# Kernel tuning notes

Measured on AMD Instinct MI355X. Metric: run time of the kernel, lower is better.

Reference implementation:

```python
import jax, jax.numpy as jnp
import numpy as np

TEXT_SIZE = 1024
HIDDEN = 512

def setup_inputs() -> dict:
    key = jax.random.key(0)
    k1, k2, k3, k4, k5, k6 = jax.random.split(key, 6)
    B, S, D, H = 32, 4096, TEXT_SIZE, HIDDEN
    text_seq = jax.random.normal(k1, (B, S, D), dtype=jnp.float32)
    previous_hidden = jax.random.normal(k2, (B, D), dtype=jnp.float32)
    # attention_hidden: Linear(D -> H) + ReLU
    W1 = jax.random.normal(k3, (D, H), dtype=jnp.float32) / np.sqrt(D)
    b1 = jax.random.normal(k4, (H,), dtype=jnp.float32) * 0.01
    # attention_scoring: Linear(H -> 1)
    w2 = jax.random.normal(k5, (H,), dtype=jnp.float32) / np.sqrt(H)
    b2 = jax.random.normal(k6, (), dtype=jnp.float32) * 0.01
    return {"text_seq": text_seq, "previous_hidden": previous_hidden,
            "W1": W1, "b1": b1, "w2": w2, "b2": b2}

def reference(text_seq, previous_hidden, W1, b1, w2, b2):
    # text_seq: [B, S, D]; previous_hidden: [B, D]
    # per-timestep: score = Linear1(ReLU(Linear0(prev * h_t))) -> batched here
    prod = text_seq * previous_hidden[:, None, :]          # [B, S, D]
    hidden = jax.nn.relu(jnp.einsum('bsd,dh->bsh', prod, W1) + b1)  # [B, S, H]
    scores = jnp.einsum('bsh,h->bs', hidden, w2) + b2      # [B, S]
    weights = jax.nn.softmax(scores, axis=1)               # [B, S]
    out = jnp.einsum('bsd,bs->bd', text_seq, weights)      # [B, D]
    return out
```

## Files before the change

### kernel.cpp

```cpp
#include <hip/hip_runtime.h>
#include <hip/hip_bf16.h>
#include <stdint.h>

#define B_ 32
#define S_ 4096
#define D_ 1024
#define H_ 512
#define BK 32
#define NCHUNK 64

typedef __bf16 bf16_t;
typedef bf16_t bf16x8 __attribute__((ext_vector_type(8)));
typedef float f32x4 __attribute__((ext_vector_type(4)));

#define AS_STRIDE 40

__global__ __launch_bounds__(256)
void ta_prep_kernel(const float* __restrict__ W1, bf16_t* __restrict__ W1bf)
{
    const int kb = blockIdx.x;
    const int t  = threadIdx.x;

#pragma unroll
    for (int hh = 0; hh < 2; ++hh) {
        int h = t + hh * 256;
        bf16_t row[BK];
#pragma unroll
        for (int kk = 0; kk < BK; ++kk)
            row[kk] = (bf16_t)W1[(size_t)(kb * BK + kk) * H_ + h];
        bf16_t* dst = W1bf + ((size_t)kb * H_ + h) * BK;
#pragma unroll
        for (int c = 0; c < 4; ++c)
            *(bf16x8*)(dst + c * 8) = *(const bf16x8*)&row[c * 8];
    }
}

__global__ __launch_bounds__(256, 2)
void ta_fused_kernel(const float* __restrict__ x,
                     const float* __restrict__ prev,
                     const bf16_t* __restrict__ W1bf,
                     const float* __restrict__ b1,
                     const float* __restrict__ w2,
                     const float* __restrict__ b2,
                     float* __restrict__ pout,
                     float* __restrict__ mlbuf)
{
    __shared__ bf16_t As[64 * AS_STRIDE];
    __shared__ bf16_t Bs[H_ * BK];
    __shared__ float  scoreS[4][64];
    __shared__ float  wS[64];

    const int t    = threadIdx.x;
    const int wv   = t >> 6;
    const int lane = t & 63;
    const int quad = lane >> 4;
    const int n16  = lane & 15;

    const int b  = blockIdx.y;
    const int s0 = blockIdx.x * 64;

    const int ar = t >> 2;
    const int ac = (t & 3) * 8;
    const float* xrow  = x + ((size_t)b * S_ + s0 + ar) * D_;
    const float* prevb = prev + (size_t)b * D_;

    float b1v[8], w2v[8];
#pragma unroll
    for (int j = 0; j < 8; ++j) {
        int h = wv * 128 + j * 16 + n16;
        b1v[j] = b1[h];
        w2v[j] = w2[h];
    }

    f32x4 acc[4][8];
#pragma unroll
    for (int i = 0; i < 4; ++i)
#pragma unroll
        for (int j = 0; j < 8; ++j)
            acc[i][j] = (f32x4){0.f, 0.f, 0.f, 0.f};

    for (int kb = 0; kb < D_ / BK; ++kb) {
        f32x4 a0 = *(const f32x4*)(xrow + kb * BK + ac);
        f32x4 a1 = *(const f32x4*)(xrow + kb * BK + ac + 4);
        f32x4 p0 = *(const f32x4*)(prevb + kb * BK + ac);
        f32x4 p1 = *(const f32x4*)(prevb + kb * BK + ac + 4);

        __syncthreads();

        const char* gB = (const char*)(W1bf + (size_t)kb * H_ * BK);
#pragma unroll
        for (int r = 0; r < 8; ++r) {
            int off = (wv * 8 + r) * 1024;
            __builtin_amdgcn_global_load_lds(
                (const __attribute__((address_space(1))) void*)(gB + off + lane * 16),
                (__attribute__((address_space(3))) void*)((char*)Bs + off),
                16, 0, 0);
        }

        {
            a0 *= p0;
            a1 *= p1;
            bf16x8 aw;
#pragma unroll
            for (int e = 0; e < 4; ++e) { aw[e] = (bf16_t)a0[e]; aw[4 + e] = (bf16_t)a1[e]; }
            *(bf16x8*)&As[ar * AS_STRIDE + ac] = aw;
        }

        __syncthreads();

        bf16x8 afr[4];
#pragma unroll
        for (int i = 0; i < 4; ++i)
            afr[i] = *(const bf16x8*)&As[(i * 16 + n16) * AS_STRIDE + quad * 8];
#pragma unroll
        for (int j = 0; j < 8; ++j) {
            bf16x8 bfr = *(const bf16x8*)&Bs[(wv * 128 + j * 16 + n16) * BK + quad * 8];
#pragma unroll
            for (int i = 0; i < 4; ++i)
                acc[i][j] = __builtin_amdgcn_mfma_f32_16x16x32_bf16(afr[i], bfr, acc[i][j], 0, 0, 0);
        }
    }

    float part[4][4];
#pragma unroll
    for (int i = 0; i < 4; ++i)
#pragma unroll
        for (int r = 0; r < 4; ++r) {
            float p = 0.f;
#pragma unroll
            for (int j = 0; j < 8; ++j) {
                float hval = acc[i][j][r] + b1v[j];
                hval = fmaxf(hval, 0.f);
                p += hval * w2v[j];
            }
            for (int off = 8; off > 0; off >>= 1)
                p += __shfl_xor(p, off);
            part[i][r] = p;
        }

    if (n16 == 0) {
#pragma unroll
        for (int i = 0; i < 4; ++i)
#pragma unroll
            for (int r = 0; r < 4; ++r)
                scoreS[wv][i * 16 + quad * 4 + r] = part[i][r];
    }
    __syncthreads();

    if (t < 64) {
        float sc = scoreS[0][t] + scoreS[1][t] + scoreS[2][t] + scoreS[3][t] + b2[0];
        float m = sc;
#pragma unroll
        for (int off = 32; off > 0; off >>= 1)
            m = fmaxf(m, __shfl_xor(m, off));
        float wexp = __expf(sc - m);
        float l = wexp;
#pragma unroll
        for (int off = 32; off > 0; off >>= 1)
            l += __shfl_xor(l, off);
        wS[t] = wexp;
        if (t == 0) {
            float* ml = mlbuf + ((size_t)b * NCHUNK + blockIdx.x) * 2;
            ml[0] = m;
            ml[1] = l;
        }
    }
    __syncthreads();

    const float* xb = x + ((size_t)b * S_ + s0) * D_;
    f32x4 acc0 = (f32x4){0.f,0.f,0.f,0.f}, acc1 = acc0, acc2 = acc0, acc3 = acc0;
    for (int s = 0; s < 64; s += 4) {
        f32x4 x0 = *(const f32x4*)(xb + (size_t)(s + 0) * D_ + t * 4);
        f32x4 x1 = *(const f32x4*)(xb + (size_t)(s + 1) * D_ + t * 4);
        f32x4 x2 = *(const f32x4*)(xb + (size_t)(s + 2) * D_ + t * 4);
        f32x4 x3 = *(const f32x4*)(xb + (size_t)(s + 3) * D_ + t * 4);
        acc0 += x0 * wS[s + 0];
        acc1 += x1 * wS[s + 1];
        acc2 += x2 * wS[s + 2];
        acc3 += x3 * wS[s + 3];
    }
    f32x4 r = (acc0 + acc1) + (acc2 + acc3);
    *(f32x4*)(pout + ((size_t)b * NCHUNK + blockIdx.x) * D_ + t * 4) = r;
}

__global__ __launch_bounds__(256)
void ta_combine_kernel(const float* __restrict__ pout,
                       const float* __restrict__ mlbuf,
                       float* __restrict__ out)
{
    const int b = blockIdx.y;
    const int t = threadIdx.x;
    const int d = blockIdx.x * 256 + t;

    __shared__ float scaleS[NCHUNK];
    if (t < NCHUNK) {
        const float* ml = mlbuf + ((size_t)b * NCHUNK + t) * 2;
        float m = ml[0];
        float l = ml[1];
        float M = m;
#pragma unroll
        for (int off = 32; off > 0; off >>= 1)
            M = fmaxf(M, __shfl_xor(M, off));
        float le = l * __expf(m - M);
        float L = le;
#pragma unroll
        for (int off = 32; off > 0; off >>= 1)
            L += __shfl_xor(L, off);
        scaleS[t] = __expf(m - M) / L;
    }
    __syncthreads();

    const float* pb = pout + (size_t)b * NCHUNK * D_ + d;
    float a0 = 0.f, a1 = 0.f, a2 = 0.f, a3 = 0.f;
#pragma unroll 4
    for (int c = 0; c < NCHUNK; c += 4) {
        a0 += pb[(size_t)(c + 0) * D_] * scaleS[c + 0];
        a1 += pb[(size_t)(c + 1) * D_] * scaleS[c + 1];
        a2 += pb[(size_t)(c + 2) * D_] * scaleS[c + 2];
        a3 += pb[(size_t)(c + 3) * D_] * scaleS[c + 3];
    }
    out[(size_t)b * D_ + d] = (a0 + a1) + (a2 + a3);
}

extern "C" void kernel_launch(void* const* d_in, const int* in_sizes, int n_in,
                              void* d_out, int out_size, void* d_ws, size_t ws_size,
                              hipStream_t stream) {
    const float* x    = (const float*)d_in[0];
    const float* prev = (const float*)d_in[1];
    const float* W1   = (const float*)d_in[2];
    const float* b1   = (const float*)d_in[3];
    const float* w2   = (const float*)d_in[4];
    const float* b2   = (const float*)d_in[5];
    float* out = (float*)d_out;

    bf16_t* W1bf  = (bf16_t*)d_ws;
    float*  pout  = (float*)((char*)d_ws + (size_t)1 * 1024 * 1024);
    float*  mlbuf = (float*)((char*)d_ws + (size_t)9 * 1024 * 1024);

    ta_prep_kernel<<<32, 256, 0, stream>>>(W1, W1bf);

    dim3 g1(NCHUNK, B_);
    ta_fused_kernel<<<g1, 256, 0, stream>>>(x, prev, W1bf, b1, w2, b2, pout, mlbuf);

    dim3 g2(D_ / 256, B_);
    ta_combine_kernel<<<g2, 256, 0, stream>>>(pout, mlbuf, out);
}
```

Measured before the change: 838.8 us.

## Double-buffer A/B tiles and prefetch x two steps ahead in fused GEMM

Restructures the K-loop into a software pipeline. A and B LDS tiles are double-buffered, the next W1 tile is issued via global_load_lds while MFMAs run on the current one, and x rows are register-prefetched two iterations ahead. prev is staged once in shared memory instead of reloaded from global each step, and one barrier per iteration replaces two. This raises LDS use, which may limit occupancy, and adds hand-written waitcnt/barrier asm that must match the load counts.

After: 830.6 us. Within noise of the previous version (-1.0%).

```diff
diff --git a/kernel.cpp b/kernel.cpp
--- a/kernel.cpp
+++ b/kernel.cpp
@@ -45,8 +45,9 @@
                      float* __restrict__ pout,
                      float* __restrict__ mlbuf)
 {
-    __shared__ bf16_t As[64 * AS_STRIDE];
-    __shared__ bf16_t Bs[H_ * BK];
+    __shared__ bf16_t As[2][64 * AS_STRIDE];
+    __shared__ bf16_t Bs[2][H_ * BK];
+    __shared__ float  prevS[D_];
     __shared__ float  scoreS[4][64];
     __shared__ float  wS[64];
 
@@ -64,61 +65,106 @@
     const float* xrow  = x + ((size_t)b * S_ + s0 + ar) * D_;
     const float* prevb = prev + (size_t)b * D_;
 
+    f32x4 acc[4][8];
+#pragma unroll
+    for (int i = 0; i < 4; ++i)
+#pragma unroll
+        for (int j = 0; j < 8; ++j)
+            acc[i][j] = (f32x4){0.f, 0.f, 0.f, 0.f};
+
+    *(f32x4*)&prevS[t * 4] = *(const f32x4*)(prevb + t * 4);
+
+    f32x4 xA0 = *(const f32x4*)(xrow + ac);
+    f32x4 xA1 = *(const f32x4*)(xrow + ac + 4);
+
+    {
+        const char* gB = (const char*)W1bf;
+#pragma unroll
+        for (int r = 0; r < 8; ++r) {
+            int off = (wv * 8 + r) * 1024;
+            __builtin_amdgcn_global_load_lds(
+                (const __attribute__((address_space(1))) void*)(gB + off + lane * 16),
+                (__attribute__((address_space(3))) void*)((char*)Bs[0] + off),
+                16, 0, 0);
+        }
+    }
+    __syncthreads();
+
+    {
+        f32x4 pv0 = *(const f32x4*)&prevS[ac];
+        f32x4 pv1 = *(const f32x4*)&prevS[ac + 4];
+        f32x4 sc0 = xA0 * pv0, sc1 = xA1 * pv1;
+        bf16x8 aw;
+#pragma unroll
+        for (int e = 0; e < 4; ++e) { aw[e] = (bf16_t)sc0[e]; aw[4 + e] = (bf16_t)sc1[e]; }
+        *(bf16x8*)&As[0][ar * AS_STRIDE + ac] = aw;
+    }
+    f32x4 xB0 = *(const f32x4*)(xrow + BK + ac);
+    f32x4 xB1 = *(const f32x4*)(xrow + BK + ac + 4);
+
+    asm volatile("s_waitcnt lgkmcnt(0)\n\ts_barrier" ::: "memory");
+
+#define TA_BODY(KB, CBUF, XU0, XU1, XN0, XN1)                                    \
+    {                                                                            \
+        const int kb_ = (KB);                                                    \
+        bf16x8 afr[4];                                                           \
+        _Pragma("unroll")                                                        \
+        for (int i = 0; i < 4; ++i)                                              \
+            afr[i] = *(const bf16x8*)&As[CBUF][(i * 16 + n16) * AS_STRIDE + quad * 8]; \
+               \
+        {                                                                        \
+            const int kp = (kb_ + 1 < 32) ? kb_ + 1 : 31;                        \
+            f32x4 pv0 = *(const f32x4*)&prevS[kp * BK + ac];                     \
+            f32x4 pv1 = *(const f32x4*)&prevS[kp * BK + ac + 4];                 \
+            f32x4 sc0 = XU0 * pv0, sc1 = XU1 * pv1;                              \
+            bf16x8 aw;                                                           \
+            _Pragma("unroll")                                                    \
+            for (int e = 0; e < 4; ++e) { aw[e] = (bf16_t)sc0[e]; aw[4 + e] = (bf16_t)sc1[e]; } \
+            *(bf16x8*)&As[(CBUF) ^ 1][ar * AS_STRIDE + ac] = aw;                 \
+        }                                                                        \
+                       \
+        {                                                                        \
+            const int kp = (kb_ + 1 < 32) ? kb_ + 1 : 31;                        \
+            const char* gB = (const char*)(W1bf + (size_t)kp * H_ * BK);         \
+            char* lB = (char*)Bs[(CBUF) ^ 1];                                    \
+            _Pragma("unroll")                                                    \
+            for (int r = 0; r < 8; ++r) {                                        \
+                int off = (wv * 8 + r) * 1024;                                   \
+                __builtin_amdgcn_global_load_lds(                                \
+                    (const __attribute__((address_space(1))) void*)(gB + off + lane * 16), \
+                    (__attribute__((address_space(3))) void*)(lB + off), 16, 0, 0); \
+            }                                                                    \
+        }                                                                        \
+                    \
+        {                                                                        \
+            const int kp2 = (kb_ + 2 < 32) ? kb_ + 2 : 31;                       \
+            XN0 = *(const f32x4*)(xrow + kp2 * BK + ac);                         \
+            XN1 = *(const f32x4*)(xrow + kp2 * BK + ac + 4);                     \
+        }                                                                        \
+                \
+        _Pragma("unroll")                                                        \
+        for (int j = 0; j < 8; ++j) {                                            \
+            bf16x8 bfr = *(const bf16x8*)&Bs[CBUF][(wv * 128 + j * 16 + n16) * BK + quad * 8]; \
+            _Pragma("unroll")                                                    \
+            for (int i = 0; i < 4; ++i)                                          \
+                acc[i][j] = __builtin_amdgcn_mfma_f32_16x16x32_bf16(afr[i], bfr, acc[i][j], 0, 0, 0); \
+        }                                                                        \
+                    \
+        asm volatile("s_waitcnt vmcnt(2) lgkmcnt(0)\n\ts_barrier" ::: "memory"); \
+    }
+
+    for (int kb2 = 0; kb2 < 32; kb2 += 2) {
+        TA_BODY(kb2,     0, xB0, xB1, xA0, xA1);
+        TA_BODY(kb2 + 1, 1, xA0, xA1, xB0, xB1);
+    }
+#undef TA_BODY
+
     float b1v[8], w2v[8];
 #pragma unroll
     for (int j = 0; j < 8; ++j) {
         int h = wv * 128 + j * 16 + n16;
         b1v[j] = b1[h];
         w2v[j] = w2[h];
-    }
-
-    f32x4 acc[4][8];
-#pragma unroll
-    for (int i = 0; i < 4; ++i)
-#pragma unroll
-        for (int j = 0; j < 8; ++j)
-            acc[i][j] = (f32x4){0.f, 0.f, 0.f, 0.f};
-
-    for (int kb = 0; kb < D_ / BK; ++kb) {
-        f32x4 a0 = *(const f32x4*)(xrow + kb * BK + ac);
-        f32x4 a1 = *(const f32x4*)(xrow + kb * BK + ac + 4);
-        f32x4 p0 = *(const f32x4*)(prevb + kb * BK + ac);
-        f32x4 p1 = *(const f32x4*)(prevb + kb * BK + ac + 4);
-
-        __syncthreads();
-
-        const char* gB = (const char*)(W1bf + (size_t)kb * H_ * BK);
-#pragma unroll
-        for (int r = 0; r < 8; ++r) {
-            int off = (wv * 8 + r) * 1024;
-            __builtin_amdgcn_global_load_lds(
-                (const __attribute__((address_space(1))) void*)(gB + off + lane * 16),
-                (__attribute__((address_space(3))) void*)((char*)Bs + off),
-                16, 0, 0);
-        }
-
-        {
-            a0 *= p0;
-            a1 *= p1;
-            bf16x8 aw;
-#pragma unroll
-            for (int e = 0; e < 4; ++e) { aw[e] = (bf16_t)a0[e]; aw[4 + e] = (bf16_t)a1[e]; }
-            *(bf16x8*)&As[ar * AS_STRIDE + ac] = aw;
-        }
-
-        __syncthreads();
-
-        bf16x8 afr[4];
-#pragma unroll
-        for (int i = 0; i < 4; ++i)
-            afr[i] = *(const bf16x8*)&As[(i * 16 + n16) * AS_STRIDE + quad * 8];
-#pragma unroll
-        for (int j = 0; j < 8; ++j) {
-            bf16x8 bfr = *(const bf16x8*)&Bs[(wv * 128 + j * 16 + n16) * BK + quad * 8];
-#pragma unroll
-            for (int i = 0; i < 4; ++i)
-                acc[i][j] = __builtin_amdgcn_mfma_f32_16x16x32_bf16(afr[i], bfr, acc[i][j], 0, 0, 0);
-        }
     }
 
     float part[4][4];
```
